# Kernel tuning notes

Hardware: AMD Instinct MI355X
Metric: run time of the kernel (lower is better)

The kernel has to match this reference:

```python
import jax, jax.numpy as jnp
import numpy as np

UNITS = 4096
INPUT_DIM = 1024
N = 16384


def setup_inputs() -> dict:
    key = jax.random.key(0)
    k1, k2 = jax.random.split(key)
    inputs = jax.random.normal(k1, (N, INPUT_DIM), dtype=jnp.float32)
    # Keras 'random_normal' initializer: stddev 0.05
    w = jax.random.normal(k2, (UNITS, INPUT_DIM), dtype=jnp.float32) * 0.05
    return {"inputs": inputs, "w": w}


def reference(inputs, w):
    # Pairwise squared Euclidean distance: out[n, u] = sum_d (w[u,d] - x[n,d])^2
    x_sq = jnp.sum(inputs * inputs, axis=-1, keepdims=True)        # [N, 1]
    w_sq = jnp.sum(w * w, axis=-1)                                  # [U]
    cross = jnp.einsum("nd,ud->nu", inputs, w)                     # [N, U]
    return x_sq + w_sq[None, :] - 2.0 * cross
```

## Files before the change

kernel.cpp:

```cpp
#include <hip/hip_runtime.h>
#include <cstdint>
#include <cstddef>

#define AS1 __attribute__((address_space(1)))
#define AS3 __attribute__((address_space(3)))

typedef unsigned int u32;
typedef unsigned char u8;
typedef int i32x4 __attribute__((ext_vector_type(4)));
typedef int i32x8 __attribute__((ext_vector_type(8)));
typedef float f32x4 __attribute__((ext_vector_type(4)));

constexpr int D  = 1024;
constexpr int NS = 16384;
constexpr int US = 4096;
constexpr int BM = 256, BN = 256, BK = 128;
constexpr int KT = D / BK;

constexpr size_t XQ_OFF  = 0;
constexpr size_t WQ_OFF  = (size_t)NS * D;
constexpr size_t XSQ_OFF = WQ_OFF + (size_t)US * D;
constexpr size_t WSQ_OFF = XSQ_OFF + (size_t)NS * 4;

__global__ __launch_bounds__(256) void quant_sq(
    const float* __restrict__ x, const float* __restrict__ w,
    u8* __restrict__ xq, u8* __restrict__ wq,
    float* __restrict__ xsq, float* __restrict__ wsq) {
  const int lane = threadIdx.x & 63;
  const int wave = blockIdx.x * 4 + (threadIdx.x >> 6);
  const int nwaves = gridDim.x * 4;
  for (int row = wave; row < NS + US; row += nwaves) {
    const float* src; u8* qdst; float* sdst; int r; float qscale;
    if (row < NS) { src = x; qdst = xq; sdst = xsq; r = row; qscale = 1.0f; }
    else          { src = w; qdst = wq; sdst = wsq; r = row - NS; qscale = 16.0f; }
    const float4* s4 = (const float4*)(src + (size_t)r * D);
    u32* qrow = (u32*)(qdst + (size_t)r * D);
    float s = 0.f;
#pragma unroll
    for (int it = 0; it < 4; ++it) {
      const float4 v = s4[it * 64 + lane];
      s += v.x * v.x + v.y * v.y + v.z * v.z + v.w * v.w;
      u32 p01 = __builtin_amdgcn_cvt_pk_fp8_f32(v.x * qscale, v.y * qscale, 0, false);
      u32 w0  = __builtin_amdgcn_cvt_pk_fp8_f32(v.z * qscale, v.w * qscale, p01, true);
      qrow[it * 64 + lane] = w0;
    }
#pragma unroll
    for (int off = 32; off; off >>= 1) s += __shfl_down(s, off, 64);
    if (lane == 0) sdst[r] = s;
  }
}

__global__ __launch_bounds__(512, 2) void dist_gemm(
    const u8* __restrict__ xq, const u8* __restrict__ wq,
    const float* __restrict__ xsq, const float* __restrict__ wsq,
    float* __restrict__ out) {
  __shared__ u8 lds[2 * 65536];

  const int tid = threadIdx.x;
  const int lane = tid & 63;
  const int wv = tid >> 6;
  const int wm = wv >> 2;
  const int wn = wv & 3;
  const int quad = lane >> 4;
  const int l15 = lane & 15;

  const int m0 = blockIdx.y * BM;
  const int n0 = blockIdx.x * BN;

  const int srow = tid >> 3;
  const int sch = lane & 7;

  f32x4 acc[8][4];
#pragma unroll
  for (int mt = 0; mt < 8; ++mt)
#pragma unroll
    for (int nt = 0; nt < 4; ++nt) acc[mt][nt] = (f32x4){0.f, 0.f, 0.f, 0.f};

  auto stageA = [&](int buf, int kt, int sw) {
    const int r = sw * 64 + srow;
    const int cg = sch ^ (r & 7);
    const u8* g = xq + (size_t)(m0 + r) * D + kt * BK + cg * 16;
    __builtin_amdgcn_global_load_lds((AS1 void*)(u8*)g,
        (AS3 void*)(lds + buf * 65536 + sw * 8192 + wv * 1024), 16, 0, 0);
  };
  auto stageB = [&](int buf, int kt, int sw) {
    const int r = sw * 64 + srow;
    const int cg = sch ^ (r & 7);
    const u8* g = wq + (size_t)(n0 + r) * D + kt * BK + cg * 16;
    __builtin_amdgcn_global_load_lds((AS1 void*)(u8*)g,
        (AS3 void*)(lds + buf * 65536 + 32768 + sw * 8192 + wv * 1024), 16, 0, 0);
  };
  auto ldfrag = [&](const u8* mat, int row) -> i32x8 {
    const int s = row & 7;
    const i32x4 f0 = *reinterpret_cast<const i32x4*>(mat + row * BK + ((2 * quad) ^ s) * 16);
    const i32x4 f1 = *reinterpret_cast<const i32x4*>(mat + row * BK + ((2 * quad + 1) ^ s) * 16);
    return __builtin_shufflevector(f0, f1, 0, 1, 2, 3, 4, 5, 6, 7);
  };

#pragma unroll
  for (int sw = 0; sw < 4; ++sw) stageA(0, 0, sw);
#pragma unroll
  for (int sw = 0; sw < 4; ++sw) stageB(0, 0, sw);
#pragma unroll
  for (int sw = 0; sw < 4; ++sw) stageA(1, 1, sw);
#pragma unroll
  for (int sw = 0; sw < 4; ++sw) stageB(1, 1, sw);
  asm volatile("s_waitcnt vmcnt(8)" ::: "memory");
  __builtin_amdgcn_sched_barrier(0);
  __builtin_amdgcn_s_barrier();
  __builtin_amdgcn_sched_barrier(0);

#define MM(MT, NT, AF) \
  acc[MT][NT] = __builtin_amdgcn_mfma_scale_f32_16x16x128_f8f6f4( \
      AF, bf[NT], acc[MT][NT], 0, 0, 0, 0x7F7F7F7F, 0, 0x7F7F7F7F)

#define OPEN_PHASE() do { \
    __builtin_amdgcn_sched_barrier(0); \
    __builtin_amdgcn_s_barrier(); \
    asm volatile("s_waitcnt lgkmcnt(0)" ::: "memory"); \
    __builtin_amdgcn_sched_barrier(0); \
    __builtin_amdgcn_s_setprio(1); } while (0)

#define CLOSE_PHASE() do { \
    __builtin_amdgcn_s_setprio(0); \
    __builtin_amdgcn_sched_barrier(0); \
    __builtin_amdgcn_s_barrier(); \
    __builtin_amdgcn_sched_barrier(0); } while (0)

#pragma unroll
  for (int t = 0; t < KT; ++t) {
    const u8* sA = lds + (t & 1) * 65536;
    const u8* sB = sA + 32768;
    const int nb = (t + 1) & 1;
    const int ar = wm * 128 + l15;
    const int br = wn * 64 + l15;

    i32x8 bf[4];

    {
      bf[0] = ldfrag(sB, br);
      bf[1] = ldfrag(sB, br + 16);
      bf[2] = ldfrag(sB, br + 32);
      bf[3] = ldfrag(sB, br + 48);
      i32x8 a0 = ldfrag(sA, ar);
      i32x8 a1 = ldfrag(sA, ar + 16);
      if (t >= 1 && t + 1 < KT) { stageA(nb, t + 1, 1); stageA(nb, t + 1, 3); }
      OPEN_PHASE();
      MM(0, 0, a0); MM(0, 1, a0); MM(0, 2, a0); MM(0, 3, a0);
      MM(1, 0, a1); MM(1, 1, a1); MM(1, 2, a1); MM(1, 3, a1);
      CLOSE_PHASE();
    }
    {
      i32x8 a0 = ldfrag(sA, ar + 32);
      i32x8 a1 = ldfrag(sA, ar + 48);
      if (t + 2 < KT) { stageB(t & 1, t + 2, 0); stageB(t & 1, t + 2, 1); stageB(t & 1, t + 2, 2); }
      OPEN_PHASE();
      MM(2, 0, a0); MM(2, 1, a0); MM(2, 2, a0); MM(2, 3, a0);
      MM(3, 0, a1); MM(3, 1, a1); MM(3, 2, a1); MM(3, 3, a1);
      CLOSE_PHASE();
    }
    {
      i32x8 a0 = ldfrag(sA, ar + 64);
      i32x8 a1 = ldfrag(sA, ar + 80);
      if (t + 2 < KT) { stageB(t & 1, t + 2, 3); stageA(t & 1, t + 2, 0); stageA(t & 1, t + 2, 2); }
      OPEN_PHASE();
      MM(4, 0, a0); MM(4, 1, a0); MM(4, 2, a0); MM(4, 3, a0);
      MM(5, 0, a1); MM(5, 1, a1); MM(5, 2, a1); MM(5, 3, a1);
      CLOSE_PHASE();
    }
    {
      i32x8 a0 = ldfrag(sA, ar + 96);
      i32x8 a1 = ldfrag(sA, ar + 112);
      OPEN_PHASE();
      MM(6, 0, a0); MM(6, 1, a0); MM(6, 2, a0); MM(6, 3, a0);
      MM(7, 0, a1); MM(7, 1, a1); MM(7, 2, a1); MM(7, 3, a1);
      __builtin_amdgcn_s_setprio(0);
      __builtin_amdgcn_sched_barrier(0);
      if (t < KT - 1) {
        if (t + 2 < KT) asm volatile("s_waitcnt vmcnt(6)" ::: "memory");
        else            asm volatile("s_waitcnt vmcnt(0)" ::: "memory");
        __builtin_amdgcn_sched_barrier(0);
        __builtin_amdgcn_s_barrier();
        __builtin_amdgcn_sched_barrier(0);
      }
    }
  }

#pragma unroll
  for (int mt = 0; mt < 8; ++mt) {
    const int R0 = m0 + wm * 128 + mt * 16 + quad * 4;
#pragma unroll
    for (int nt = 0; nt < 4; ++nt) {
      const int C = n0 + wn * 64 + nt * 16 + l15;
      const float wsv = wsq[C];
#pragma unroll
      for (int r = 0; r < 4; ++r) {
        const int R = R0 + r;
        out[(size_t)R * US + C] = xsq[R] + wsv - 0.125f * acc[mt][nt][r];
      }
    }
  }
}

extern "C" void kernel_launch(void* const* d_in, const int* in_sizes, int n_in,
                              void* d_out, int out_size, void* d_ws, size_t ws_size,
                              hipStream_t stream) {
  const float* x = (const float*)d_in[0];
  const float* w = (const float*)d_in[1];
  float* out = (float*)d_out;
  char* ws = (char*)d_ws;

  u8* xq = (u8*)(ws + XQ_OFF);
  u8* wq = (u8*)(ws + WQ_OFF);
  float* xsq = (float*)(ws + XSQ_OFF);
  float* wsq = (float*)(ws + WSQ_OFF);

  quant_sq<<<dim3(640), dim3(256), 0, stream>>>(x, w, xq, wq, xsq, wsq);
  dist_gemm<<<dim3(US / BN, NS / BM), dim3(512), 0, stream>>>(xq, wq, xsq, wsq, out);
}
```

Measured before the change: 383.1 us.

## Peel last K-tile to overlap epilogue stores with MFMAs and refine prologue waits

Peels the final K iteration out of the main loop and interleaves the output stores for finished row-tiles with the remaining MFMA phases, so epilogue writes overlap with compute. Reorders the prologue loads so the first A halves and B arrive first, and relaxes the initial vmcnt wait so compute can start before all of tile 0 is resident. Also doubles the grid of the quantize kernel. This hides part of the store tail and startup latency, at the cost of more complex wait counts that must stay correct.

```diff
diff --git a/kernel.cpp b/kernel.cpp
--- a/kernel.cpp
+++ b/kernel.cpp
@@ -97,15 +97,15 @@
     return __builtin_shufflevector(f0, f1, 0, 1, 2, 3, 4, 5, 6, 7);
   };
 
-#pragma unroll
-  for (int sw = 0; sw < 4; ++sw) stageA(0, 0, sw);
+  stageA(0, 0, 0); stageA(0, 0, 2);
 #pragma unroll
   for (int sw = 0; sw < 4; ++sw) stageB(0, 0, sw);
+  stageA(0, 0, 1); stageA(0, 0, 3);
 #pragma unroll
   for (int sw = 0; sw < 4; ++sw) stageA(1, 1, sw);
 #pragma unroll
   for (int sw = 0; sw < 4; ++sw) stageB(1, 1, sw);
-  asm volatile("s_waitcnt vmcnt(8)" ::: "memory");
+  asm volatile("s_waitcnt vmcnt(10)" ::: "memory");
   __builtin_amdgcn_sched_barrier(0);
   __builtin_amdgcn_s_barrier();
   __builtin_amdgcn_sched_barrier(0);
@@ -128,7 +128,7 @@
     __builtin_amdgcn_sched_barrier(0); } while (0)
 
 #pragma unroll
-  for (int t = 0; t < KT; ++t) {
+  for (int t = 0; t < KT - 1; ++t) {
     const u8* sA = lds + (t & 1) * 65536;
     const u8* sB = sA + 32768;
     const int nb = (t + 1) & 1;
@@ -144,7 +144,7 @@
       bf[3] = ldfrag(sB, br + 48);
       i32x8 a0 = ldfrag(sA, ar);
       i32x8 a1 = ldfrag(sA, ar + 16);
-      if (t >= 1 && t + 1 < KT) { stageA(nb, t + 1, 1); stageA(nb, t + 1, 3); }
+      if (t >= 1) { stageA(nb, t + 1, 1); stageA(nb, t + 1, 3); }
       OPEN_PHASE();
       MM(0, 0, a0); MM(0, 1, a0); MM(0, 2, a0); MM(0, 3, a0);
       MM(1, 0, a1); MM(1, 1, a1); MM(1, 2, a1); MM(1, 3, a1);
@@ -160,6 +160,10 @@
       CLOSE_PHASE();
     }
     {
+      if (t == 0) {
+        asm volatile("s_waitcnt vmcnt(11)" ::: "memory");
+        __builtin_amdgcn_sched_barrier(0);
+      }
       i32x8 a0 = ldfrag(sA, ar + 64);
       i32x8 a1 = ldfrag(sA, ar + 80);
       if (t + 2 < KT) { stageB(t & 1, t + 2, 3); stageA(t & 1, t + 2, 0); stageA(t & 1, t + 2, 2); }
@@ -176,29 +180,84 @@
       MM(7, 0, a1); MM(7, 1, a1); MM(7, 2, a1); MM(7, 3, a1);
       __builtin_amdgcn_s_setprio(0);
       __builtin_amdgcn_sched_barrier(0);
-      if (t < KT - 1) {
-        if (t + 2 < KT) asm volatile("s_waitcnt vmcnt(6)" ::: "memory");
-        else            asm volatile("s_waitcnt vmcnt(0)" ::: "memory");
-        __builtin_amdgcn_sched_barrier(0);
-        __builtin_amdgcn_s_barrier();
-        __builtin_amdgcn_sched_barrier(0);
+      if (t + 2 < KT) asm volatile("s_waitcnt vmcnt(6)" ::: "memory");
+      else            asm volatile("s_waitcnt vmcnt(0)" ::: "memory");
+      __builtin_amdgcn_sched_barrier(0);
+      __builtin_amdgcn_s_barrier();
+      __builtin_amdgcn_sched_barrier(0);
+    }
+  }
+
+  {
+    const u8* sA = lds + 65536;
+    const u8* sB = sA + 32768;
+    const int ar = wm * 128 + l15;
+    const int br = wn * 64 + l15;
+
+    float wsv[4];
+#pragma unroll
+    for (int nt = 0; nt < 4; ++nt) wsv[nt] = wsq[n0 + wn * 64 + nt * 16 + l15];
+
+    i32x8 bf[4];
+    bf[0] = ldfrag(sB, br);
+    bf[1] = ldfrag(sB, br + 16);
+    bf[2] = ldfrag(sB, br + 32);
+    bf[3] = ldfrag(sB, br + 48);
+
+    auto xs_of = [&](int mt) -> f32x4 {
+      return *reinterpret_cast<const f32x4*>(xsq + m0 + wm * 128 + mt * 16 + quad * 4);
+    };
+    auto store2 = [&](int mt, const f32x4 xs) {
+      const int R0 = m0 + wm * 128 + mt * 16 + quad * 4;
+#pragma unroll
+      for (int nt = 0; nt < 4; ++nt) {
+        const int C = n0 + wn * 64 + nt * 16 + l15;
+#pragma unroll
+        for (int r = 0; r < 4; ++r)
+          out[(size_t)(R0 + r) * US + C] = xs[r] + wsv[nt] - 0.125f * acc[mt][nt][r];
       }
-    }
-  }
-
-#pragma unroll
-  for (int mt = 0; mt < 8; ++mt) {
-    const int R0 = m0 + wm * 128 + mt * 16 + quad * 4;
-#pragma unroll
-    for (int nt = 0; nt < 4; ++nt) {
-      const int C = n0 + wn * 64 + nt * 16 + l15;
-      const float wsv = wsq[C];
-#pragma unroll
-      for (int r = 0; r < 4; ++r) {
-        const int R = R0 + r;
-        out[(size_t)R * US + C] = xsq[R] + wsv - 0.125f * acc[mt][nt][r];
-      }
-    }
+    };
+
+    f32x4 xs0 = xs_of(0), xs1 = xs_of(1);
+    {
+      i32x8 a0 = ldfrag(sA, ar);
+      i32x8 a1 = ldfrag(sA, ar + 16);
+      __builtin_amdgcn_s_setprio(1);
+      MM(0, 0, a0); MM(0, 1, a0); MM(0, 2, a0); MM(0, 3, a0);
+      MM(1, 0, a1); MM(1, 1, a1); MM(1, 2, a1); MM(1, 3, a1);
+      __builtin_amdgcn_s_setprio(0);
+    }
+    f32x4 xs2 = xs_of(2), xs3 = xs_of(3);
+    {
+      i32x8 a0 = ldfrag(sA, ar + 32);
+      i32x8 a1 = ldfrag(sA, ar + 48);
+      __builtin_amdgcn_s_setprio(1);
+      MM(2, 0, a0); MM(2, 1, a0); MM(2, 2, a0); MM(2, 3, a0);
+      MM(3, 0, a1); MM(3, 1, a1); MM(3, 2, a1); MM(3, 3, a1);
+      __builtin_amdgcn_s_setprio(0);
+    }
+    store2(0, xs0); store2(1, xs1);
+    f32x4 xs4 = xs_of(4), xs5 = xs_of(5);
+    {
+      i32x8 a0 = ldfrag(sA, ar + 64);
+      i32x8 a1 = ldfrag(sA, ar + 80);
+      __builtin_amdgcn_s_setprio(1);
+      MM(4, 0, a0); MM(4, 1, a0); MM(4, 2, a0); MM(4, 3, a0);
+      MM(5, 0, a1); MM(5, 1, a1); MM(5, 2, a1); MM(5, 3, a1);
+      __builtin_amdgcn_s_setprio(0);
+    }
+    store2(2, xs2); store2(3, xs3);
+    f32x4 xs6 = xs_of(6), xs7 = xs_of(7);
+    {
+      i32x8 a0 = ldfrag(sA, ar + 96);
+      i32x8 a1 = ldfrag(sA, ar + 112);
+      __builtin_amdgcn_s_setprio(1);
+      MM(6, 0, a0); MM(6, 1, a0); MM(6, 2, a0); MM(6, 3, a0);
+      MM(7, 0, a1); MM(7, 1, a1); MM(7, 2, a1); MM(7, 3, a1);
+      __builtin_amdgcn_s_setprio(0);
+    }
+    store2(4, xs4); store2(5, xs5);
+    store2(6, xs6); store2(7, xs7);
   }
 }
 
@@ -215,6 +274,6 @@
   float* xsq = (float*)(ws + XSQ_OFF);
   float* wsq = (float*)(ws + WSQ_OFF);
 
-  quant_sq<<<dim3(640), dim3(256), 0, stream>>>(x, w, xq, wq, xsq, wsq);
+  quant_sq<<<dim3(1280), dim3(256), 0, stream>>>(x, w, xq, wq, xsq, wsq);
   dist_gemm<<<dim3(US / BN, NS / BM), dim3(512), 0, stream>>>(xq, wq, xsq, wsq, out);
 }
```

After: 376.9 us. No clear change (-1.6%).

## Shrink GEMM tile to 128x128 with 4 waves and a simpler double-buffered loop

Applied to the files above, without the earlier changes.

Reduces the block tile from 256x256 with 8 waves to 128x128 with 4 waves. The four-phase interleaved staging schedule is replaced by a plain double buffer: prefetch the next K tile, run all 16 MFMAs, then wait and barrier. The epilogue now loads the row norms as a vector, and the quantization grid is doubled. Smaller tiles give more blocks and less LDS per block, but they also lower data reuse and expose more load latency per K step.

```diff
diff --git a/kernel.cpp b/kernel.cpp
--- a/kernel.cpp
+++ b/kernel.cpp
@@ -14,7 +14,7 @@
 constexpr int D  = 1024;
 constexpr int NS = 16384;
 constexpr int US = 4096;
-constexpr int BM = 256, BN = 256, BK = 128;
+constexpr int BM = 128, BN = 128, BK = 128;
 constexpr int KT = D / BK;
 
 constexpr size_t XQ_OFF  = 0;
@@ -50,17 +50,17 @@
   }
 }
 
-__global__ __launch_bounds__(512, 2) void dist_gemm(
+__global__ __launch_bounds__(256, 2) void dist_gemm(
     const u8* __restrict__ xq, const u8* __restrict__ wq,
     const float* __restrict__ xsq, const float* __restrict__ wsq,
     float* __restrict__ out) {
-  __shared__ u8 lds[2 * 65536];
+  __shared__ u8 lds[2 * 32768];
 
   const int tid = threadIdx.x;
   const int lane = tid & 63;
   const int wv = tid >> 6;
-  const int wm = wv >> 2;
-  const int wn = wv & 3;
+  const int wm = wv >> 1;
+  const int wn = wv & 1;
   const int quad = lane >> 4;
   const int l15 = lane & 15;
 
@@ -70,25 +70,25 @@
   const int srow = tid >> 3;
   const int sch = lane & 7;
 
-  f32x4 acc[8][4];
+  f32x4 acc[4][4];
 #pragma unroll
-  for (int mt = 0; mt < 8; ++mt)
+  for (int mt = 0; mt < 4; ++mt)
 #pragma unroll
     for (int nt = 0; nt < 4; ++nt) acc[mt][nt] = (f32x4){0.f, 0.f, 0.f, 0.f};
 
   auto stageA = [&](int buf, int kt, int sw) {
-    const int r = sw * 64 + srow;
+    const int r = sw * 32 + srow;
     const int cg = sch ^ (r & 7);
     const u8* g = xq + (size_t)(m0 + r) * D + kt * BK + cg * 16;
     __builtin_amdgcn_global_load_lds((AS1 void*)(u8*)g,
-        (AS3 void*)(lds + buf * 65536 + sw * 8192 + wv * 1024), 16, 0, 0);
+        (AS3 void*)(lds + buf * 32768 + sw * 4096 + wv * 1024), 16, 0, 0);
   };
   auto stageB = [&](int buf, int kt, int sw) {
-    const int r = sw * 64 + srow;
+    const int r = sw * 32 + srow;
     const int cg = sch ^ (r & 7);
     const u8* g = wq + (size_t)(n0 + r) * D + kt * BK + cg * 16;
     __builtin_amdgcn_global_load_lds((AS1 void*)(u8*)g,
-        (AS3 void*)(lds + buf * 65536 + 32768 + sw * 8192 + wv * 1024), 16, 0, 0);
+        (AS3 void*)(lds + buf * 32768 + 16384 + sw * 4096 + wv * 1024), 16, 0, 0);
   };
   auto ldfrag = [&](const u8* mat, int row) -> i32x8 {
     const int s = row & 7;
@@ -97,107 +97,79 @@
     return __builtin_shufflevector(f0, f1, 0, 1, 2, 3, 4, 5, 6, 7);
   };
 
-#pragma unroll
-  for (int sw = 0; sw < 4; ++sw) stageA(0, 0, sw);
-#pragma unroll
-  for (int sw = 0; sw < 4; ++sw) stageB(0, 0, sw);
-#pragma unroll
-  for (int sw = 0; sw < 4; ++sw) stageA(1, 1, sw);
-#pragma unroll
-  for (int sw = 0; sw < 4; ++sw) stageB(1, 1, sw);
-  asm volatile("s_waitcnt vmcnt(8)" ::: "memory");
-  __builtin_amdgcn_sched_barrier(0);
-  __builtin_amdgcn_s_barrier();
-  __builtin_amdgcn_sched_barrier(0);
+  const int ar = wm * 64 + l15;
+  const int br = wn * 64 + l15;
 
 #define MM(MT, NT, AF) \
   acc[MT][NT] = __builtin_amdgcn_mfma_scale_f32_16x16x128_f8f6f4( \
       AF, bf[NT], acc[MT][NT], 0, 0, 0, 0x7F7F7F7F, 0, 0x7F7F7F7F)
 
-#define OPEN_PHASE() do { \
-    __builtin_amdgcn_sched_barrier(0); \
-    __builtin_amdgcn_s_barrier(); \
-    asm volatile("s_waitcnt lgkmcnt(0)" ::: "memory"); \
-    __builtin_amdgcn_sched_barrier(0); \
-    __builtin_amdgcn_s_setprio(1); } while (0)
+#define SB() __builtin_amdgcn_sched_barrier(0)
 
-#define CLOSE_PHASE() do { \
-    __builtin_amdgcn_s_setprio(0); \
-    __builtin_amdgcn_sched_barrier(0); \
-    __builtin_amdgcn_s_barrier(); \
-    __builtin_amdgcn_sched_barrier(0); } while (0)
+#pragma unroll
+  for (int sw = 0; sw < 4; ++sw) stageA(0, 0, sw);
+#pragma unroll
+  for (int sw = 0; sw < 4; ++sw) stageB(0, 0, sw);
+  asm volatile("s_waitcnt vmcnt(0)" ::: "memory");
+  SB();
+  __builtin_amdgcn_s_barrier();
+  SB();
 
 #pragma unroll
   for (int t = 0; t < KT; ++t) {
-    const u8* sA = lds + (t & 1) * 65536;
-    const u8* sB = sA + 32768;
+    const u8* sA = lds + (t & 1) * 32768;
+    const u8* sB = sA + 16384;
     const int nb = (t + 1) & 1;
-    const int ar = wm * 128 + l15;
-    const int br = wn * 64 + l15;
+
+    if (t + 1 < KT) {
+#pragma unroll
+      for (int sw = 0; sw < 4; ++sw) stageA(nb, t + 1, sw);
+#pragma unroll
+      for (int sw = 0; sw < 4; ++sw) stageB(nb, t + 1, sw);
+    }
 
     i32x8 bf[4];
+    bf[0] = ldfrag(sB, br);
+    bf[1] = ldfrag(sB, br + 16);
+    bf[2] = ldfrag(sB, br + 32);
+    bf[3] = ldfrag(sB, br + 48);
+    i32x8 a0 = ldfrag(sA, ar);
+    i32x8 a1 = ldfrag(sA, ar + 16);
+    i32x8 a2 = ldfrag(sA, ar + 32);
+    i32x8 a3 = ldfrag(sA, ar + 48);
 
-    {
-      bf[0] = ldfrag(sB, br);
-      bf[1] = ldfrag(sB, br + 16);
-      bf[2] = ldfrag(sB, br + 32);
-      bf[3] = ldfrag(sB, br + 48);
-      i32x8 a0 = ldfrag(sA, ar);
-      i32x8 a1 = ldfrag(sA, ar + 16);
-      if (t >= 1 && t + 1 < KT) { stageA(nb, t + 1, 1); stageA(nb, t + 1, 3); }
-      OPEN_PHASE();
-      MM(0, 0, a0); MM(0, 1, a0); MM(0, 2, a0); MM(0, 3, a0);
-      MM(1, 0, a1); MM(1, 1, a1); MM(1, 2, a1); MM(1, 3, a1);
-      CLOSE_PHASE();
-    }
-    {
-      i32x8 a0 = ldfrag(sA, ar + 32);
-      i32x8 a1 = ldfrag(sA, ar + 48);
-      if (t + 2 < KT) { stageB(t & 1, t + 2, 0); stageB(t & 1, t + 2, 1); stageB(t & 1, t + 2, 2); }
-      OPEN_PHASE();
-      MM(2, 0, a0); MM(2, 1, a0); MM(2, 2, a0); MM(2, 3, a0);
-      MM(3, 0, a1); MM(3, 1, a1); MM(3, 2, a1); MM(3, 3, a1);
-      CLOSE_PHASE();
-    }
-    {
-      i32x8 a0 = ldfrag(sA, ar + 64);
-      i32x8 a1 = ldfrag(sA, ar + 80);
-      if (t + 2 < KT) { stageB(t & 1, t + 2, 3); stageA(t & 1, t + 2, 0); stageA(t & 1, t + 2, 2); }
-      OPEN_PHASE();
-      MM(4, 0, a0); MM(4, 1, a0); MM(4, 2, a0); MM(4, 3, a0);
-      MM(5, 0, a1); MM(5, 1, a1); MM(5, 2, a1); MM(5, 3, a1);
-      CLOSE_PHASE();
-    }
-    {
-      i32x8 a0 = ldfrag(sA, ar + 96);
-      i32x8 a1 = ldfrag(sA, ar + 112);
-      OPEN_PHASE();
-      MM(6, 0, a0); MM(6, 1, a0); MM(6, 2, a0); MM(6, 3, a0);
-      MM(7, 0, a1); MM(7, 1, a1); MM(7, 2, a1); MM(7, 3, a1);
-      __builtin_amdgcn_s_setprio(0);
-      __builtin_amdgcn_sched_barrier(0);
-      if (t < KT - 1) {
-        if (t + 2 < KT) asm volatile("s_waitcnt vmcnt(6)" ::: "memory");
-        else            asm volatile("s_waitcnt vmcnt(0)" ::: "memory");
-        __builtin_amdgcn_sched_barrier(0);
-        __builtin_amdgcn_s_barrier();
-        __builtin_amdgcn_sched_barrier(0);
-      }
+    asm volatile("s_waitcnt lgkmcnt(0)" ::: "memory");
+    SB();
+    __builtin_amdgcn_s_setprio(1);
+    MM(0, 0, a0); MM(0, 1, a0); MM(0, 2, a0); MM(0, 3, a0);
+    MM(1, 0, a1); MM(1, 1, a1); MM(1, 2, a1); MM(1, 3, a1);
+    MM(2, 0, a2); MM(2, 1, a2); MM(2, 2, a2); MM(2, 3, a2);
+    MM(3, 0, a3); MM(3, 1, a3); MM(3, 2, a3); MM(3, 3, a3);
+    __builtin_amdgcn_s_setprio(0);
+    SB();
+
+    if (t + 1 < KT) {
+      asm volatile("s_waitcnt vmcnt(0)" ::: "memory");
+      SB();
+      __builtin_amdgcn_s_barrier();
+      SB();
     }
   }
 
+  float wsv[4];
 #pragma unroll
-  for (int mt = 0; mt < 8; ++mt) {
-    const int R0 = m0 + wm * 128 + mt * 16 + quad * 4;
+  for (int nt = 0; nt < 4; ++nt) wsv[nt] = wsq[n0 + wn * 64 + nt * 16 + l15];
+
+#pragma unroll
+  for (int mt = 0; mt < 4; ++mt) {
+    const int R0 = m0 + wm * 64 + mt * 16 + quad * 4;
+    const f32x4 xs = *reinterpret_cast<const f32x4*>(xsq + R0);
 #pragma unroll
     for (int nt = 0; nt < 4; ++nt) {
       const int C = n0 + wn * 64 + nt * 16 + l15;
-      const float wsv = wsq[C];
 #pragma unroll
-      for (int r = 0; r < 4; ++r) {
-        const int R = R0 + r;
-        out[(size_t)R * US + C] = xsq[R] + wsv - 0.125f * acc[mt][nt][r];
-      }
+      for (int r = 0; r < 4; ++r)
+        out[(size_t)(R0 + r) * US + C] = xs[r] + wsv[nt] - 0.125f * acc[mt][nt][r];
     }
   }
 }
@@ -215,6 +187,6 @@
   float* xsq = (float*)(ws + XSQ_OFF);
   float* wsq = (float*)(ws + WSQ_OFF);
 
-  quant_sq<<<dim3(640), dim3(256), 0, stream>>>(x, w, xq, wq, xsq, wsq);
-  dist_gemm<<<dim3(US / BN, NS / BM), dim3(512), 0, stream>>>(xq, wq, xsq, wsq, out);
+  quant_sq<<<dim3(1280), dim3(256), 0, stream>>>(x, w, xq, wq, xsq, wsq);
+  dist_gemm<<<dim3(US / BN, NS / BM), dim3(256), 0, stream>>>(xq, wq, xsq, wsq, out);
 }
```

Result: faster. 373.2 us (-2.6%).
